# Kernel tuning notes

Measured on AMD Instinct MI355X. Metric: run time of the kernel, lower is better.

## Reference

```python
import jax, jax.numpy as jnp
import numpy as np

MIN_NORM = 1e-15
PROJ_EPS = 4e-3  # fp32 eps used by hgcn PoincareBall


def _artanh(x):
    x = jnp.clip(x, -1.0 + 1e-7, 1.0 - 1e-7)
    return 0.5 * jnp.log((1.0 + x) / (1.0 - x))


def _norm(x):
    return jnp.maximum(jnp.linalg.norm(x, axis=-1, keepdims=True), MIN_NORM)


def proj(x, c):
    norm = _norm(x)
    maxnorm = (1.0 - PROJ_EPS) / jnp.sqrt(c)
    return jnp.where(norm > maxnorm, x / norm * maxnorm, x)


def expmap0(u, c):
    sqrt_c = jnp.sqrt(c)
    u_norm = _norm(u)
    return jnp.tanh(sqrt_c * u_norm) * u / (sqrt_c * u_norm)


def logmap0(p, c):
    sqrt_c = jnp.sqrt(c)
    p_norm = _norm(p)
    return _artanh(sqrt_c * p_norm) * p / (sqrt_c * p_norm)


def mobius_add(x, y, c):
    x2 = jnp.sum(x * x, axis=-1, keepdims=True)
    y2 = jnp.sum(y * y, axis=-1, keepdims=True)
    xy = jnp.sum(x * y, axis=-1, keepdims=True)
    num = (1.0 + 2.0 * c * xy + c * y2) * x + (1.0 - c * x2) * y
    denom = 1.0 + 2.0 * c * xy + c * c * x2 * y2
    return num / jnp.maximum(denom, MIN_NORM)


def mobius_matvec(m, x, c):
    sqrt_c = jnp.sqrt(c)
    x_norm = _norm(x)
    mx = x @ m.T  # [N, out]
    mx_norm = _norm(mx)
    res_c = jnp.tanh(mx_norm / x_norm * _artanh(sqrt_c * x_norm)) * mx / (mx_norm * sqrt_c)
    cond = jnp.all(mx == 0.0, axis=-1, keepdims=True)
    return jnp.where(cond, jnp.zeros_like(res_c), res_c)


def setup_inputs() -> dict:
    key = jax.random.key(0)
    k1, k2, k3 = jax.random.split(key, 3)
    N, D = 8192, 256
    c = 1.0
    x = 0.05 * jax.random.normal(k1, (N, D), dtype=jnp.float32)
    x = proj(x, c)  # valid points on the Poincare ball
    # sparse-ish row-normalized adjacency, materialized densely
    a = (jax.random.uniform(k2, (N, N)) < 0.004).astype(jnp.float32)
    a = a + jnp.eye(N, dtype=jnp.float32)
    adj = a / jnp.sum(a, axis=-1, keepdims=True)
    gain = np.sqrt(2.0)
    bound = gain * np.sqrt(6.0 / (D + D))  # xavier_uniform with gain sqrt(2)
    weight = jax.random.uniform(k3, (D, D), minval=-bound, maxval=bound, dtype=jnp.float32)
    bias = jnp.zeros((D,), dtype=jnp.float32)
    return {"x": x, "adj": adj, "weight": weight, "bias": bias}


def reference(x, adj, weight, bias):
    c_in = jnp.float32(1.0)
    c_out = jnp.float32(1.0)
    # HypLinear (dropout=0, eval mode)
    mv = mobius_matvec(weight, x, c_in)
    res = proj(mv, c_in)
    hyp_bias = proj(expmap0(bias[None, :], c_in), c_in)  # proj_tan0 is identity
    h = proj(mobius_add(res, hyp_bias, c_in), c_in)
    # HypAgg (use_att=False): tangent-space neighborhood aggregation
    x_tangent = logmap0(h, c_in)
    support_t = adj @ x_tangent
    h = proj(expmap0(support_t, c_in), c_in)
    # HypAct
    xt = jax.nn.relu(logmap0(h, c_in))
    h = proj(expmap0(xt, c_out), c_out)
    return (h, adj)
```

## Files before the change

### kernel.cpp

```cpp
#include <hip/hip_runtime.h>
#include <hip/hip_bf16.h>

#define N_NODES 8192
#define D_DIM   256

typedef __attribute__((ext_vector_type(8))) short short8v;
typedef __attribute__((ext_vector_type(4))) float f32x4;

__device__ __forceinline__ float artanh_clip(float x) {
    x = fminf(x, 1.0f - 1e-7f);
    return 0.5f * logf((1.0f + x) / (1.0f - x));
}

__device__ __forceinline__ ushort4 cvt4_bf16(float4 v) {
    ushort4 b;
    b.x = __bfloat16_as_ushort(__float2bfloat16(v.x));
    b.y = __bfloat16_as_ushort(__float2bfloat16(v.y));
    b.z = __bfloat16_as_ushort(__float2bfloat16(v.z));
    b.w = __bfloat16_as_ushort(__float2bfloat16(v.w));
    return b;
}

__device__ __forceinline__ void nt_store4(float4 v, float* p) {
    f32x4 w = {v.x, v.y, v.z, v.w};
    __builtin_nontemporal_store(w, (f32x4*)p);
}

__global__ void k0_bias(const float* __restrict__ bias, float* __restrict__ hbg) {
    __shared__ float sp[4];
    __shared__ float s_g;
    int t = threadIdx.x;
    float u = bias[t];
    float v = u * u;
    #pragma unroll
    for (int o = 1; o < 64; o <<= 1) v += __shfl_xor(v, o);
    if ((t & 63) == 0) sp[t >> 6] = v;
    __syncthreads();
    if (t == 0) {
        float s  = sp[0] + sp[1] + sp[2] + sp[3];
        float un = fmaxf(sqrtf(s), 1e-15f);
        float t1 = tanhf(un);
        s_g = (t1 > 0.996f) ? (0.996f / un) : (t1 / un);
    }
    __syncthreads();
    float hb = s_g * u;
    hbg[t] = hb;
    float v2 = hb * hb;
    #pragma unroll
    for (int o = 1; o < 64; o <<= 1) v2 += __shfl_xor(v2, o);
    if ((t & 63) == 0) sp[t >> 6] = v2;
    __syncthreads();
    if (t == 0) hbg[256] = sp[0] + sp[1] + sp[2] + sp[3];
}

__global__ __launch_bounds__(256) void k1_hyplinear(
    const float* __restrict__ x, const float* __restrict__ W,
    const float* __restrict__ hbg, __hip_bfloat16* __restrict__ xtT)
{
    __shared__ __align__(16) float sx[16][264];
    __shared__ __align__(16) float sw[256][36];
    __shared__ float s_xn[16], s_P[16], s_Q[16];
    __shared__ float s_hb[256];
    __shared__ float s_b2;

    const int t  = threadIdx.x;
    const int r0 = blockIdx.x * 16;
    const int row = t >> 4;
    const int j16 = (t & 15) * 4;

    {
        #pragma unroll
        for (int i = 0; i < 4; i++)
            *(float4*)(&sx[row][j16 + 64 * i]) =
                *(const float4*)(x + (r0 + row) * 256 + j16 + 64 * i);
    }
    s_hb[t] = hbg[t];
    if (t == 0) s_b2 = hbg[256];
    __syncthreads();

    {
        int r = t >> 4, j = t & 15;
        float s2 = 0.f;
        #pragma unroll
        for (int i = 0; i < 16; i++) { float v = sx[r][j + 16 * i]; s2 += v * v; }
        s2 += __shfl_xor(s2, 1); s2 += __shfl_xor(s2, 2);
        s2 += __shfl_xor(s2, 4); s2 += __shfl_xor(s2, 8);
        if (j == 0) s_xn[r] = s2;
    }

    float acc[16];
    #pragma unroll
    for (int r = 0; r < 16; r++) acc[r] = 0.f;

    for (int kc = 0; kc < 8; kc++) {
        __syncthreads();
        {
            int c4 = (t & 7) * 4;
            #pragma unroll
            for (int i = 0; i < 8; i++) {
                int d = i * 32 + (t >> 3);
                *(float4*)(&sw[d][c4]) = *(const float4*)(W + d * 256 + kc * 32 + c4);
            }
        }
        __syncthreads();
        #pragma unroll
        for (int kk = 0; kk < 8; kk++) {
            float4 w4 = *(const float4*)(&sw[t][kk * 4]);
            #pragma unroll
            for (int r = 0; r < 16; r++) {
                float4 x4 = *(const float4*)(&sx[r][kc * 32 + kk * 4]);
                acc[r] = fmaf(x4.x, w4.x, acc[r]);
                acc[r] = fmaf(x4.y, w4.y, acc[r]);
                acc[r] = fmaf(x4.z, w4.z, acc[r]);
                acc[r] = fmaf(x4.w, w4.w, acc[r]);
            }
        }
    }
    __syncthreads();
    #pragma unroll
    for (int r = 0; r < 16; r++) sx[r][t] = acc[r];
    __syncthreads();

    {
        int r = t >> 4, j = t & 15;
        float s2 = 0.f, dt = 0.f;
        #pragma unroll
        for (int i = 0; i < 16; i++) {
            float v = sx[r][j + 16 * i];
            s2 += v * v;
            dt += v * s_hb[j + 16 * i];
        }
        s2 += __shfl_xor(s2, 1); s2 += __shfl_xor(s2, 2);
        s2 += __shfl_xor(s2, 4); s2 += __shfl_xor(s2, 8);
        dt += __shfl_xor(dt, 1); dt += __shfl_xor(dt, 2);
        dt += __shfl_xor(dt, 4); dt += __shfl_xor(dt, 8);
        if (j == 0) {
            float b2  = s_b2;
            float xn  = fmaxf(sqrtf(s_xn[r]), 1e-15f);
            float mx2 = s2;
            float mxn = fmaxf(sqrtf(mx2), 1e-15f);
            float at = artanh_clip(xn);
            float tt = tanhf(mxn / xn * at);
            float fr = tt / mxn;
            if (tt > 0.996f) fr = 0.996f / mxn;
            float mvn = fminf(tt, 0.996f);
            float x2  = mvn * mvn;
            float xy  = fr * dt;
            float cA  = 1.0f + 2.0f * xy + b2;
            float cB  = 1.0f - x2;
            float den = fmaxf(1.0f + 2.0f * xy + x2 * b2, 1e-15f);
            float P0 = cA * fr / den;
            float Q0 = cB / den;
            float hn = sqrtf(fmaxf(P0 * P0 * mx2 + 2.0f * P0 * Q0 * dt + Q0 * Q0 * b2, 0.0f));
            hn = fmaxf(hn, 1e-15f);
            float pf  = (hn > 0.996f) ? (0.996f / hn) : 1.0f;
            float hnp = fminf(hn, 0.996f);
            float lam = artanh_clip(hnp) / hnp;
            s_P[r] = lam * pf * P0;
            s_Q[r] = lam * pf * Q0;
        }
    }
    __syncthreads();

    {
        float hb = s_hb[t];
        unsigned int pk[8];
        #pragma unroll
        for (int r = 0; r < 16; r += 2) {
            float a0 = s_P[r]     * acc[r]     + s_Q[r]     * hb;
            float a1 = s_P[r + 1] * acc[r + 1] + s_Q[r + 1] * hb;
            unsigned int lo = (unsigned int)__bfloat16_as_ushort(__float2bfloat16(a0));
            unsigned int hi = (unsigned int)__bfloat16_as_ushort(__float2bfloat16(a1));
            pk[r >> 1] = lo | (hi << 16);
        }
        uint4* dst = (uint4*)(xtT + t * 8192 + r0);
        dst[0] = make_uint4(pk[0], pk[1], pk[2], pk[3]);
        dst[1] = make_uint4(pk[4], pk[5], pk[6], pk[7]);
    }
}

__global__ __launch_bounds__(256) void k2_agg(
    const float* __restrict__ adj,
    const __hip_bfloat16* __restrict__ xtT,
    float* __restrict__ out_h,
    float* __restrict__ out_adj)
{
    __shared__ __align__(16) __hip_bfloat16 As[2][16][72];

    const int t    = threadIdx.x;
    const int lane = t & 63;
    const int wave = t >> 6;
    const int m0   = blockIdx.x * 16;

    const int srow  = t >> 4;
    const int sslot = t & 15;
    const float* aptr = adj     + (m0 + srow) * 8192 + sslot * 4;
    float*       optr = out_adj + (m0 + srow) * 8192 + sslot * 4;

    const int arow = lane & 15;
    const int g8   = 8 * (lane >> 4);
    const __hip_bfloat16* bbase = xtT + (wave * 64 + arow) * 8192 + g8;

    f32x4 acc[4];
    #pragma unroll
    for (int i = 0; i < 4; i++) acc[i] = (f32x4){0.f, 0.f, 0.f, 0.f};

    float4 Ta, Tb;
    Ta = *(const float4*)(aptr);
    Tb = *(const float4*)(aptr + 64);
    nt_store4(Ta, optr);
    *(ushort4*)(&As[0][srow][sslot * 4]) = cvt4_bf16(Ta);
    __syncthreads();

    for (int kt = 0; kt < 128; kt += 2) {
        {
            short8v B[4][2];
            #pragma unroll
            for (int nf = 0; nf < 4; nf++)
                #pragma unroll
                for (int ks = 0; ks < 2; ks++)
                    B[nf][ks] = *(const short8v*)(bbase + nf * 16 * 8192 + kt * 64 + ks * 32);
            if (kt + 2 < 128) Ta = *(const float4*)(aptr + (kt + 2) * 64);

            short8v a0 = *(const short8v*)(&As[0][arow][g8]);
            short8v a1 = *(const short8v*)(&As[0][arow][32 + g8]);
            #pragma unroll
            for (int nf = 0; nf < 4; nf++) {
                acc[nf] = __builtin_amdgcn_mfma_f32_16x16x32_bf16(a0, B[nf][0], acc[nf], 0, 0, 0);
                acc[nf] = __builtin_amdgcn_mfma_f32_16x16x32_bf16(a1, B[nf][1], acc[nf], 0, 0, 0);
            }
            nt_store4(Tb, optr + (kt + 1) * 64);
            *(ushort4*)(&As[1][srow][sslot * 4]) = cvt4_bf16(Tb);
            __syncthreads();
        }
        {
            short8v B[4][2];
            #pragma unroll
            for (int nf = 0; nf < 4; nf++)
                #pragma unroll
                for (int ks = 0; ks < 2; ks++)
                    B[nf][ks] = *(const short8v*)(bbase + nf * 16 * 8192 + (kt + 1) * 64 + ks * 32);
            if (kt + 3 < 128) Tb = *(const float4*)(aptr + (kt + 3) * 64);

            short8v a0 = *(const short8v*)(&As[1][arow][g8]);
            short8v a1 = *(const short8v*)(&As[1][arow][32 + g8]);
            #pragma unroll
            for (int nf = 0; nf < 4; nf++) {
                acc[nf] = __builtin_amdgcn_mfma_f32_16x16x32_bf16(a0, B[nf][0], acc[nf], 0, 0, 0);
                acc[nf] = __builtin_amdgcn_mfma_f32_16x16x32_bf16(a1, B[nf][1], acc[nf], 0, 0, 0);
            }
            if (kt + 2 < 128) {
                nt_store4(Ta, optr + (kt + 2) * 64);
                *(ushort4*)(&As[0][srow][sslot * 4]) = cvt4_bf16(Ta);
            }
            __syncthreads();
        }
    }

    const int crow0 = 4 * (lane >> 4);
    const int ccol  = lane & 15;
    #pragma unroll
    for (int nf = 0; nf < 4; nf++)
        #pragma unroll
        for (int q = 0; q < 4; q++)
            out_h[(m0 + crow0 + q) * 256 + wave * 64 + nf * 16 + ccol] = acc[nf][q];
}

__global__ __launch_bounds__(256) void k3_epilogue(float* __restrict__ h) {
    const int t = threadIdx.x;
    const int r = blockIdx.x * 16 + (t >> 4);
    const int j = t & 15;
    float* p = h + r * 256 + j * 16;

    float4 v[4];
    float s2 = 0.f, sp = 0.f;
    #pragma unroll
    for (int i = 0; i < 4; i++) {
        v[i] = *(const float4*)(p + 4 * i);
        s2 += v[i].x * v[i].x + v[i].y * v[i].y + v[i].z * v[i].z + v[i].w * v[i].w;
        float px = fmaxf(v[i].x, 0.f), py = fmaxf(v[i].y, 0.f);
        float pz = fmaxf(v[i].z, 0.f), pw = fmaxf(v[i].w, 0.f);
        sp += px * px + py * py + pz * pz + pw * pw;
    }
    s2 += __shfl_xor(s2, 1); s2 += __shfl_xor(s2, 2); s2 += __shfl_xor(s2, 4); s2 += __shfl_xor(s2, 8);
    sp += __shfl_xor(sp, 1); sp += __shfl_xor(sp, 2); sp += __shfl_xor(sp, 4); sp += __shfl_xor(sp, 8);

    float ns = fmaxf(sqrtf(s2), 1e-15f);
    float t1 = tanhf(ns);
    float alpha = (t1 > 0.996f) ? (0.996f / ns) : (t1 / ns);
    float nh = fminf(t1, 0.996f);
    float beta = artanh_clip(nh) / nh;
    float ba = beta * alpha;
    float nxt = fmaxf(ba * sqrtf(sp), 1e-15f);
    float t2 = tanhf(nxt);
    float delta = (t2 > 0.996f) ? (0.996f / nxt) : (t2 / nxt);
    float F = delta * ba;

    #pragma unroll
    for (int i = 0; i < 4; i++) {
        float4 o;
        o.x = F * fmaxf(v[i].x, 0.f);
        o.y = F * fmaxf(v[i].y, 0.f);
        o.z = F * fmaxf(v[i].z, 0.f);
        o.w = F * fmaxf(v[i].w, 0.f);
        *(float4*)(p + 4 * i) = o;
    }
}

extern "C" void kernel_launch(void* const* d_in, const int* in_sizes, int n_in,
                              void* d_out, int out_size, void* d_ws, size_t ws_size,
                              hipStream_t stream)
{
    const float* x    = (const float*)d_in[0];
    const float* adj  = (const float*)d_in[1];
    const float* W    = (const float*)d_in[2];
    const float* bias = (const float*)d_in[3];

    float* out_h   = (float*)d_out;
    float* out_adj = out_h + (size_t)N_NODES * D_DIM;

    __hip_bfloat16* xtT = (__hip_bfloat16*)d_ws;
    float* hbg = (float*)((char*)d_ws + (size_t)D_DIM * N_NODES * 2);

    k0_bias<<<1, 256, 0, stream>>>(bias, hbg);
    k1_hyplinear<<<512, 256, 0, stream>>>(x, W, hbg, xtT);
    k2_agg<<<512, 256, 0, stream>>>(adj, xtT, out_h, out_adj);
    k3_epilogue<<<512, 256, 0, stream>>>(out_h);
}
```

Baseline: 378.1 us.

## Retile aggregation GEMM to 128x128 blocks with split-K partial sums

Replaces the 16-row aggregation kernel with a 128x128 output tile per block, 4x4 MFMA fragments per wave, and a four-way split over K. Partials go to a workspace buffer that the epilogue sums, with an atomic fallback when the workspace is too small. This raises MFMA reuse per loaded tile and cuts repeated reads of the transposed features. In exchange, adjacency is read twice (once per column half) and partial-sum traffic is added.

```diff
diff --git a/kernel.cpp b/kernel.cpp
--- a/kernel.cpp
+++ b/kernel.cpp
@@ -12,13 +12,10 @@
     return 0.5f * logf((1.0f + x) / (1.0f - x));
 }
 
-__device__ __forceinline__ ushort4 cvt4_bf16(float4 v) {
-    ushort4 b;
-    b.x = __bfloat16_as_ushort(__float2bfloat16(v.x));
-    b.y = __bfloat16_as_ushort(__float2bfloat16(v.y));
-    b.z = __bfloat16_as_ushort(__float2bfloat16(v.z));
-    b.w = __bfloat16_as_ushort(__float2bfloat16(v.w));
-    return b;
+__device__ __forceinline__ unsigned int pk2_bf16(float a, float b) {
+    unsigned int lo = (unsigned int)__bfloat16_as_ushort(__float2bfloat16(a));
+    unsigned int hi = (unsigned int)__bfloat16_as_ushort(__float2bfloat16(b));
+    return lo | (hi << 16);
 }
 
 __device__ __forceinline__ void nt_store4(float4 v, float* p) {
@@ -169,9 +166,7 @@
         for (int r = 0; r < 16; r += 2) {
             float a0 = s_P[r]     * acc[r]     + s_Q[r]     * hb;
             float a1 = s_P[r + 1] * acc[r + 1] + s_Q[r + 1] * hb;
-            unsigned int lo = (unsigned int)__bfloat16_as_ushort(__float2bfloat16(a0));
-            unsigned int hi = (unsigned int)__bfloat16_as_ushort(__float2bfloat16(a1));
-            pk[r >> 1] = lo | (hi << 16);
+            pk[r >> 1] = pk2_bf16(a0, a1);
         }
         uint4* dst = (uint4*)(xtT + t * 8192 + r0);
         dst[0] = make_uint4(pk[0], pk[1], pk[2], pk[3]);
@@ -179,104 +174,169 @@
     }
 }
 
-__global__ __launch_bounds__(256) void k2_agg(
+__global__ __launch_bounds__(256) void k2_gemm(
     const float* __restrict__ adj,
     const __hip_bfloat16* __restrict__ xtT,
     float* __restrict__ out_h,
-    float* __restrict__ out_adj)
+    float* __restrict__ out_adj,
+    float* __restrict__ part)
 {
-    __shared__ __align__(16) __hip_bfloat16 As[2][16][72];
+    __shared__ __align__(16) char As[2][128 * 144];
 
     const int t    = threadIdx.x;
     const int lane = t & 63;
     const int wave = t >> 6;
-    const int m0   = blockIdx.x * 16;
-
-    const int srow  = t >> 4;
-    const int sslot = t & 15;
-    const float* aptr = adj     + (m0 + srow) * 8192 + sslot * 4;
-    float*       optr = out_adj + (m0 + srow) * 8192 + sslot * 4;
-
-    const int arow = lane & 15;
-    const int g8   = 8 * (lane >> 4);
-    const __hip_bfloat16* bbase = xtT + (wave * 64 + arow) * 8192 + g8;
-
-    f32x4 acc[4];
-    #pragma unroll
-    for (int i = 0; i < 4; i++) acc[i] = (f32x4){0.f, 0.f, 0.f, 0.f};
-
-    float4 Ta, Tb;
-    Ta = *(const float4*)(aptr);
-    Tb = *(const float4*)(aptr + 64);
-    nt_store4(Ta, optr);
-    *(ushort4*)(&As[0][srow][sslot * 4]) = cvt4_bf16(Ta);
-    __syncthreads();
-
-    for (int kt = 0; kt < 128; kt += 2) {
-        {
-            short8v B[4][2];
+    const int wm   = wave >> 1;
+    const int wn   = wave & 1;
+    const int bx   = blockIdx.x;
+    const int m    = bx & 63;
+    const int j    = bx >> 6;
+    const int c    = j & 1;
+    const int s    = j >> 1;
+    const int m0   = m * 128;
+    const int n0   = c * 128;
+    const int kbase = s * 2048;
+
+    const int srow  = t >> 1;
+    const int shalf = t & 1;
+    const float* aptr = adj     + (size_t)(m0 + srow) * 8192 + kbase + shalf * 32;
+    float*       optr = out_adj + (size_t)(m0 + srow) * 8192 + kbase + shalf * 32;
+    const int sbyte = srow * 144 + shalf * 64;
+
+    const int arow16 = lane & 15;
+    const int g8     = lane >> 4;
+    const int abyte0 = (wm * 64 + arow16) * 144 + 16 * g8;
+    const __hip_bfloat16* bbase =
+        xtT + (size_t)(n0 + wn * 64 + arow16) * 8192 + kbase + 8 * g8;
+
+    f32x4 acc[4][4];
+    #pragma unroll
+    for (int i = 0; i < 4; i++)
+        #pragma unroll
+        for (int k = 0; k < 4; k++) acc[i][k] = (f32x4){0.f, 0.f, 0.f, 0.f};
+
+    float4 T[8];
+    #pragma unroll
+    for (int i = 0; i < 8; i++) T[i] = *(const float4*)(aptr + i * 4);
+    if (c == 0) {
+        #pragma unroll
+        for (int i = 0; i < 8; i++) nt_store4(T[i], optr + i * 4);
+    }
+    #pragma unroll
+    for (int i = 0; i < 4; i++) {
+        uint4 w;
+        w.x = pk2_bf16(T[2*i].x, T[2*i].y);
+        w.y = pk2_bf16(T[2*i].z, T[2*i].w);
+        w.z = pk2_bf16(T[2*i+1].x, T[2*i+1].y);
+        w.w = pk2_bf16(T[2*i+1].z, T[2*i+1].w);
+        *(uint4*)(&As[0][sbyte + i * 16]) = w;
+    }
+    __syncthreads();
+
+    int cur = 0;
+    for (int kt = 0; kt < 32; kt++) {
+        const bool hn = (kt + 1 < 32);
+        if (hn) {
+            #pragma unroll
+            for (int i = 0; i < 8; i++)
+                T[i] = *(const float4*)(aptr + (kt + 1) * 64 + i * 4);
+        }
+
+        short8v bf[4][2], af[4][2];
+        #pragma unroll
+        for (int nf = 0; nf < 4; nf++)
+            #pragma unroll
+            for (int ks = 0; ks < 2; ks++)
+                bf[nf][ks] = *(const short8v*)(bbase + (size_t)nf * 16 * 8192 + kt * 64 + ks * 32);
+        #pragma unroll
+        for (int mf = 0; mf < 4; mf++)
+            #pragma unroll
+            for (int ks = 0; ks < 2; ks++)
+                af[mf][ks] = *(const short8v*)(&As[cur][abyte0 + mf * 16 * 144 + ks * 64]);
+
+        #pragma unroll
+        for (int ks = 0; ks < 2; ks++)
+            #pragma unroll
+            for (int mf = 0; mf < 4; mf++)
+                #pragma unroll
+                for (int nf = 0; nf < 4; nf++)
+                    acc[mf][nf] = __builtin_amdgcn_mfma_f32_16x16x32_bf16(
+                        af[mf][ks], bf[nf][ks], acc[mf][nf], 0, 0, 0);
+
+        if (hn) {
+            if (c == 0) {
+                #pragma unroll
+                for (int i = 0; i < 8; i++)
+                    nt_store4(T[i], optr + (kt + 1) * 64 + i * 4);
+            }
+            #pragma unroll
+            for (int i = 0; i < 4; i++) {
+                uint4 w;
+                w.x = pk2_bf16(T[2*i].x, T[2*i].y);
+                w.y = pk2_bf16(T[2*i].z, T[2*i].w);
+                w.z = pk2_bf16(T[2*i+1].x, T[2*i+1].y);
+                w.w = pk2_bf16(T[2*i+1].z, T[2*i+1].w);
+                *(uint4*)(&As[cur ^ 1][sbyte + i * 16]) = w;
+            }
+        }
+        __syncthreads();
+        cur ^= 1;
+    }
+
+    const int crow0 = 4 * (lane >> 4);
+    const int ccol  = lane & 15;
+    if (part) {
+        float* pb = part + (size_t)s * N_NODES * D_DIM;
+        #pragma unroll
+        for (int mf = 0; mf < 4; mf++)
             #pragma unroll
             for (int nf = 0; nf < 4; nf++)
                 #pragma unroll
-                for (int ks = 0; ks < 2; ks++)
-                    B[nf][ks] = *(const short8v*)(bbase + nf * 16 * 8192 + kt * 64 + ks * 32);
-            if (kt + 2 < 128) Ta = *(const float4*)(aptr + (kt + 2) * 64);
-
-            short8v a0 = *(const short8v*)(&As[0][arow][g8]);
-            short8v a1 = *(const short8v*)(&As[0][arow][32 + g8]);
-            #pragma unroll
-            for (int nf = 0; nf < 4; nf++) {
-                acc[nf] = __builtin_amdgcn_mfma_f32_16x16x32_bf16(a0, B[nf][0], acc[nf], 0, 0, 0);
-                acc[nf] = __builtin_amdgcn_mfma_f32_16x16x32_bf16(a1, B[nf][1], acc[nf], 0, 0, 0);
-            }
-            nt_store4(Tb, optr + (kt + 1) * 64);
-            *(ushort4*)(&As[1][srow][sslot * 4]) = cvt4_bf16(Tb);
-            __syncthreads();
-        }
-        {
-            short8v B[4][2];
+                for (int q = 0; q < 4; q++)
+                    pb[(size_t)(m0 + wm * 64 + mf * 16 + crow0 + q) * 256
+                       + n0 + wn * 64 + nf * 16 + ccol] = acc[mf][nf][q];
+    } else {
+        #pragma unroll
+        for (int mf = 0; mf < 4; mf++)
             #pragma unroll
             for (int nf = 0; nf < 4; nf++)
                 #pragma unroll
-                for (int ks = 0; ks < 2; ks++)
-                    B[nf][ks] = *(const short8v*)(bbase + nf * 16 * 8192 + (kt + 1) * 64 + ks * 32);
-            if (kt + 3 < 128) Tb = *(const float4*)(aptr + (kt + 3) * 64);
-
-            short8v a0 = *(const short8v*)(&As[1][arow][g8]);
-            short8v a1 = *(const short8v*)(&As[1][arow][32 + g8]);
-            #pragma unroll
-            for (int nf = 0; nf < 4; nf++) {
-                acc[nf] = __builtin_amdgcn_mfma_f32_16x16x32_bf16(a0, B[nf][0], acc[nf], 0, 0, 0);
-                acc[nf] = __builtin_amdgcn_mfma_f32_16x16x32_bf16(a1, B[nf][1], acc[nf], 0, 0, 0);
-            }
-            if (kt + 2 < 128) {
-                nt_store4(Ta, optr + (kt + 2) * 64);
-                *(ushort4*)(&As[0][srow][sslot * 4]) = cvt4_bf16(Ta);
-            }
-            __syncthreads();
-        }
-    }
-
-    const int crow0 = 4 * (lane >> 4);
-    const int ccol  = lane & 15;
-    #pragma unroll
-    for (int nf = 0; nf < 4; nf++)
-        #pragma unroll
-        for (int q = 0; q < 4; q++)
-            out_h[(m0 + crow0 + q) * 256 + wave * 64 + nf * 16 + ccol] = acc[nf][q];
-}
-
-__global__ __launch_bounds__(256) void k3_epilogue(float* __restrict__ h) {
+                for (int q = 0; q < 4; q++)
+                    atomicAdd(out_h + (size_t)(m0 + wm * 64 + mf * 16 + crow0 + q) * 256
+                              + n0 + wn * 64 + nf * 16 + ccol, acc[mf][nf][q]);
+    }
+}
+
+__global__ __launch_bounds__(256) void k3_epilogue(
+    float* __restrict__ h, const float* __restrict__ part)
+{
     const int t = threadIdx.x;
     const int r = blockIdx.x * 16 + (t >> 4);
     const int j = t & 15;
-    float* p = h + r * 256 + j * 16;
+    float* p = h + (size_t)r * 256 + j * 16;
 
     float4 v[4];
+    if (part) {
+        const size_t base = (size_t)r * 256 + j * 16;
+        #pragma unroll
+        for (int i = 0; i < 4; i++) {
+            float4 a0 = *(const float4*)(part + base + 4 * i);
+            float4 a1 = *(const float4*)(part + (size_t)N_NODES * D_DIM + base + 4 * i);
+            float4 a2 = *(const float4*)(part + (size_t)2 * N_NODES * D_DIM + base + 4 * i);
+            float4 a3 = *(const float4*)(part + (size_t)3 * N_NODES * D_DIM + base + 4 * i);
+            v[i].x = a0.x + a1.x + a2.x + a3.x;
+            v[i].y = a0.y + a1.y + a2.y + a3.y;
+            v[i].z = a0.z + a1.z + a2.z + a3.z;
+            v[i].w = a0.w + a1.w + a2.w + a3.w;
+        }
+    } else {
+        #pragma unroll
+        for (int i = 0; i < 4; i++) v[i] = *(const float4*)(p + 4 * i);
+    }
+
     float s2 = 0.f, sp = 0.f;
     #pragma unroll
     for (int i = 0; i < 4; i++) {
-        v[i] = *(const float4*)(p + 4 * i);
         s2 += v[i].x * v[i].x + v[i].y * v[i].y + v[i].z * v[i].z + v[i].w * v[i].w;
         float px = fmaxf(v[i].x, 0.f), py = fmaxf(v[i].y, 0.f);
         float pz = fmaxf(v[i].z, 0.f), pw = fmaxf(v[i].w, 0.f);
@@ -319,11 +379,19 @@
     float* out_h   = (float*)d_out;
     float* out_adj = out_h + (size_t)N_NODES * D_DIM;
 
+    const size_t xtT_bytes = (size_t)D_DIM * N_NODES * 2;
     __hip_bfloat16* xtT = (__hip_bfloat16*)d_ws;
-    float* hbg = (float*)((char*)d_ws + (size_t)D_DIM * N_NODES * 2);
+    float* hbg = (float*)((char*)d_ws + xtT_bytes);
+
+    const size_t part_off   = xtT_bytes + 4096;
+    const size_t part_bytes = (size_t)4 * N_NODES * D_DIM * sizeof(float);
+    const bool use_part = ws_size >= part_off + part_bytes;
+    float* part = use_part ? (float*)((char*)d_ws + part_off) : nullptr;
 
     k0_bias<<<1, 256, 0, stream>>>(bias, hbg);
     k1_hyplinear<<<512, 256, 0, stream>>>(x, W, hbg, xtT);
-    k2_agg<<<512, 256, 0, stream>>>(adj, xtT, out_h, out_adj);
-    k3_epilogue<<<512, 256, 0, stream>>>(out_h);
-}
+    if (!use_part)
+        hipMemsetAsync(out_h, 0, (size_t)N_NODES * D_DIM * sizeof(float), stream);
+    k2_gemm<<<512, 256, 0, stream>>>(adj, xtT, out_h, out_adj, part);
+    k3_epilogue<<<512, 256, 0, stream>>>(out_h, part);
+}
```

New measurement: 661.6 us. 1.75x slower.
